# Optimization experiments

Measured on AMD Instinct MI355X. Metric: run time of the kernel, lower is better.

Reference implementation:

```python
import jax, jax.numpy as jnp
import numpy as np

B, S, H, D = 4, 2048, 12, 64
WINDOW = 128          # local_attention window => (w//2, w//2) sliding window
BASE = 16000.0        # rope theta (ProkBert default)
NEG = -1e9


def rotate_half(x):
    x1, x2 = jnp.split(x, 2, axis=-1)
    return jnp.concatenate([-x2, x1], axis=-1)


def setup_inputs() -> dict:
    key = jax.random.key(0)
    k1, = jax.random.split(key, 1)
    qkv = jax.random.normal(k1, (B, S, 3, H, D), dtype=jnp.float32)
    pos = jnp.arange(S)
    inv_freq = 1.0 / (BASE ** (jnp.arange(0, D, 2).astype(jnp.float32) / D))
    freqs = pos[:, None].astype(jnp.float32) * inv_freq[None, :]   # (S, D/2)
    emb = jnp.concatenate([freqs, freqs], axis=-1)                  # (S, D)
    cos = jnp.cos(emb)
    sin = jnp.sin(emb)
    dist = jnp.abs(pos[:, None] - pos[None, :])
    mask = jnp.where(dist <= WINDOW // 2, 0.0, NEG).astype(jnp.float32)[None, None]  # (1,1,S,S)
    return {"qkv": qkv, "cos": cos, "sin": sin, "mask": mask}


def reference(qkv, cos, sin, mask):
    # qkv: (B, S, 3, H, D) -> q/k/v: (B, H, S, D)
    q = jnp.swapaxes(qkv[:, :, 0], 1, 2)
    k = jnp.swapaxes(qkv[:, :, 1], 1, 2)
    v = jnp.swapaxes(qkv[:, :, 2], 1, 2)
    cos_b = cos[None, None]   # (1,1,S,D)
    sin_b = sin[None, None]
    q = q * cos_b + rotate_half(q) * sin_b
    k = k * cos_b + rotate_half(k) * sin_b
    scale = D ** -0.5
    scores = jnp.einsum('bhqd,bhkd->bhqk', q, k) * scale + mask
    w = jax.nn.softmax(scores.astype(jnp.float32), axis=-1).astype(q.dtype)
    out = jnp.einsum('bhqk,bhkd->bhqd', w, v)
    out = jnp.swapaxes(out, 1, 2).reshape(B, S, H * D)  # (B, S, dim)
    return out
```

## Files before the change

### kernel.cpp

```cpp
#include <hip/hip_runtime.h>
#include <hip/hip_bf16.h>
#include <cstdint>


typedef short bf16x8 __attribute__((ext_vector_type(8)));
typedef float f32x4  __attribute__((ext_vector_type(4)));
typedef uint32_t u32x4 __attribute__((ext_vector_type(4)));

#define SLEN   2048
#define NHEAD  12
#define NBATCH 4
#define HD     64
#define WHALF  64
#define QT     128
#define KROWS  256
#define NKC    9
#define VST    68
#define VROWS  136
#define QSCALE 0.18033688011112042f


__device__ __forceinline__ uint32_t cvt_pk(float lo, float hi) {
    uint32_t r;
    asm("v_cvt_pk_bf16_f32 %0, %1, %2" : "=v"(r) : "v"(lo), "v"(hi));
    return r;
}

__global__ __launch_bounds__(512, 6) void prokbert_attn(
        const float* __restrict__ qkv, const float* __restrict__ cosT,
        const float* __restrict__ sinT, float* __restrict__ out)
{
    __shared__ __align__(16) uint32_t sbuf[VROWS * VST];
    short* sKp = (short*)sbuf;

    const int tid = threadIdx.x;

    const int bid = blockIdx.x;
    const int gid = (bid & 7) * 96 + (bid >> 3);
    const int qt = gid & 15;
    const int hh = gid >> 4;
    const int h = hh % NHEAD, b = hh / NHEAD;

    const int q0 = qt * QT;
    const int kstart = q0 - WHALF;

    const int wv = tid >> 6;
    const int lane = tid & 63;
    const int r = lane & 15, g = lane >> 4;
    const int rx = r & 7;
    const int qrow = q0 + wv * 16 + r;

    const int rrb = tid >> 2, c4 = tid & 3, d0 = c4 * 8;

#define LOADK(IT, S) \
    f32x4 xl0##S, xl1##S, xh0##S, xh1##S, cc0##S, cc1##S, ss0##S, ss1##S; \
    { \
        const int s = kstart + rrb + (IT) * 128; \
        if ((unsigned)s < SLEN) { \
            const size_t kbase = (((size_t)(b * SLEN + s) * 3 + 1) * NHEAD + h) * HD; \
            const f32x4* gxl = (const f32x4*)(qkv + kbase + d0); \
            const f32x4* gxh = (const f32x4*)(qkv + kbase + d0 + 32); \
            const f32x4* gc  = (const f32x4*)(cosT + s * HD + d0); \
            const f32x4* gs  = (const f32x4*)(sinT + s * HD + d0); \
            xl0##S = gxl[0]; xl1##S = gxl[1]; \
            xh0##S = gxh[0]; xh1##S = gxh[1]; \
            cc0##S = gc[0];  cc1##S = gc[1]; \
            ss0##S = gs[0];  ss1##S = gs[1]; \
        } else { \
            const f32x4 z = {0.f, 0.f, 0.f, 0.f}; \
            xl0##S = z; xl1##S = z; xh0##S = z; xh1##S = z; \
            cc0##S = z; cc1##S = z; ss0##S = z; ss1##S = z; \
        } \
    }

#define CONVSTOREK(IT, S) \
    { \
        const int rr = rrb + (IT) * 128; \
        u32x4 klo, khi; \
         \
        klo[0] = cvt_pk(xl0##S[0] * cc0##S[0] - xh0##S[0] * ss0##S[0], \
                        xl0##S[1] * cc0##S[1] - xh0##S[1] * ss0##S[1]); \
        klo[1] = cvt_pk(xl0##S[2] * cc0##S[2] - xh0##S[2] * ss0##S[2], \
                        xl0##S[3] * cc0##S[3] - xh0##S[3] * ss0##S[3]); \
        klo[2] = cvt_pk(xl1##S[0] * cc1##S[0] - xh1##S[0] * ss1##S[0], \
                        xl1##S[1] * cc1##S[1] - xh1##S[1] * ss1##S[1]); \
        klo[3] = cvt_pk(xl1##S[2] * cc1##S[2] - xh1##S[2] * ss1##S[2], \
                        xl1##S[3] * cc1##S[3] - xh1##S[3] * ss1##S[3]); \
        khi[0] = cvt_pk(xh0##S[0] * cc0##S[0] + xl0##S[0] * ss0##S[0], \
                        xh0##S[1] * cc0##S[1] + xl0##S[1] * ss0##S[1]); \
        khi[1] = cvt_pk(xh0##S[2] * cc0##S[2] + xl0##S[2] * ss0##S[2], \
                        xh0##S[3] * cc0##S[3] + xl0##S[3] * ss0##S[3]); \
        khi[2] = cvt_pk(xh1##S[0] * cc1##S[0] + xl1##S[0] * ss1##S[0], \
                        xh1##S[1] * cc1##S[1] + xl1##S[1] * ss1##S[1]); \
        khi[3] = cvt_pk(xh1##S[2] * cc1##S[2] + xl1##S[2] * ss1##S[2], \
                        xh1##S[3] * cc1##S[3] + xl1##S[3] * ss1##S[3]); \
        const int sw = rr & 7; \
        *(u32x4*)&sKp[rr * 64 + ((c4 ^ sw) << 3)]       = klo; \
        *(u32x4*)&sKp[rr * 64 + (((c4 + 4) ^ sw) << 3)] = khi; \
    }

    {
        LOADK(0, a)
        LOADK(1, bb)
        CONVSTOREK(0, a)
        CONVSTOREK(1, bb)
    }
#undef LOADK
#undef CONVSTOREK

    bf16x8 qf0, qf1;
    {
        const size_t qb = (((size_t)(b * SLEN + qrow) * 3 + 0) * NHEAD + h) * HD;
        const f32x4* ga  = (const f32x4*)(qkv + qb + g * 8);
        const f32x4* gb  = (const f32x4*)(qkv + qb + 32 + g * 8);
        const f32x4* gc0 = (const f32x4*)(cosT + (size_t)qrow * HD + g * 8);
        const f32x4* gs0 = (const f32x4*)(sinT + (size_t)qrow * HD + g * 8);
        f32x4 qa0 = ga[0], qa1 = ga[1], qb0 = gb[0], qb1 = gb[1];
        f32x4 qc0 = gc0[0], qc1 = gc0[1], qs0 = gs0[0], qs1 = gs0[1];
        u32x4 w0, w1;
        w0[0] = cvt_pk((qa0[0] * qc0[0] - qb0[0] * qs0[0]) * QSCALE,
                       (qa0[1] * qc0[1] - qb0[1] * qs0[1]) * QSCALE);
        w0[1] = cvt_pk((qa0[2] * qc0[2] - qb0[2] * qs0[2]) * QSCALE,
                       (qa0[3] * qc0[3] - qb0[3] * qs0[3]) * QSCALE);
        w0[2] = cvt_pk((qa1[0] * qc1[0] - qb1[0] * qs1[0]) * QSCALE,
                       (qa1[1] * qc1[1] - qb1[1] * qs1[1]) * QSCALE);
        w0[3] = cvt_pk((qa1[2] * qc1[2] - qb1[2] * qs1[2]) * QSCALE,
                       (qa1[3] * qc1[3] - qb1[3] * qs1[3]) * QSCALE);
        w1[0] = cvt_pk((qb0[0] * qc0[0] + qa0[0] * qs0[0]) * QSCALE,
                       (qb0[1] * qc0[1] + qa0[1] * qs0[1]) * QSCALE);
        w1[1] = cvt_pk((qb0[2] * qc0[2] + qa0[2] * qs0[2]) * QSCALE,
                       (qb0[3] * qc0[3] + qa0[3] * qs0[3]) * QSCALE);
        w1[2] = cvt_pk((qb1[0] * qc1[0] + qa1[0] * qs1[0]) * QSCALE,
                       (qb1[1] * qc1[1] + qa1[1] * qs1[1]) * QSCALE);
        w1[3] = cvt_pk((qb1[2] * qc1[2] + qa1[2] * qs1[2]) * QSCALE,
                       (qb1[3] * qc1[3] + qa1[3] * qs1[3]) * QSCALE);
        qf0 = __builtin_bit_cast(bf16x8, w0);
        qf1 = __builtin_bit_cast(bf16x8, w1);
    }
    __syncthreads();

    f32x4 sc[NKC];
    #pragma unroll
    for (int kc = 0; kc < NKC; ++kc) {
        const int row = wv * 16 + kc * 16 + r;
        const bf16x8 ka0 = *(const bf16x8*)&sKp[row * 64 + ((g ^ rx) << 3)];
        const bf16x8 ka1 = *(const bf16x8*)&sKp[row * 64 + (((g + 4) ^ rx) << 3)];
        f32x4 c = {0.f, 0.f, 0.f, 0.f};
        c = __builtin_amdgcn_mfma_f32_16x16x32_bf16(ka0, qf0, c, 0, 0, 0);
        c = __builtin_amdgcn_mfma_f32_16x16x32_bf16(ka1, qf1, c, 0, 0, 0);
        sc[kc] = c;
    }

    const int tg = 4 * g;
    float sum = 0.f;
    #pragma unroll
    for (int kc = 0; kc < NKC; ++kc) {
        #pragma unroll
        for (int i = 0; i < 4; ++i) {
            float e = exp2f(sc[kc][i]);
            if (kc == 0) e = (tg + i >= r) ? e : 0.f;
            if (kc == 8) e = (tg + i <= r) ? e : 0.f;
            sc[kc][i] = e;
            sum += e;
        }
    }
    sum += __shfl_xor(sum, 16);
    sum += __shfl_xor(sum, 32);
    const int oob = max(0, WHALF - qrow) + max(0, qrow - (SLEN - 1 - WHALF));
    const float inv = 1.f / (sum - (float)oob);

    u32x4 paw[5];
    #pragma unroll
    for (int kb = 0; kb < 4; ++kb) {
        paw[kb][0] = cvt_pk(sc[2 * kb][0], sc[2 * kb][1]);
        paw[kb][1] = cvt_pk(sc[2 * kb][2], sc[2 * kb][3]);
        paw[kb][2] = cvt_pk(sc[2 * kb + 1][0], sc[2 * kb + 1][1]);
        paw[kb][3] = cvt_pk(sc[2 * kb + 1][2], sc[2 * kb + 1][3]);
    }
    paw[4][0] = cvt_pk(sc[8][0], sc[8][1]);
    paw[4][1] = cvt_pk(sc[8][2], sc[8][3]);
    paw[4][2] = 0; paw[4][3] = 0;

    const int vkp = tid >> 2, vdb = tid & 3, vd0 = vdb * 16;
    const int s0 = kstart + 2 * vkp, s1 = s0 + 1;
    f32x4 va[4], vb4[4];
    {
        const f32x4 z = {0.f, 0.f, 0.f, 0.f};
        if ((unsigned)s0 < SLEN) {
            const f32x4* g0 = (const f32x4*)(qkv +
                (((size_t)(b * SLEN + s0) * 3 + 2) * NHEAD + h) * HD + vd0);
            va[0] = g0[0]; va[1] = g0[1]; va[2] = g0[2]; va[3] = g0[3];
        } else { va[0] = z; va[1] = z; va[2] = z; va[3] = z; }
        if ((unsigned)s1 < SLEN) {
            const f32x4* g1 = (const f32x4*)(qkv +
                (((size_t)(b * SLEN + s1) * 3 + 2) * NHEAD + h) * HD + vd0);
            vb4[0] = g1[0]; vb4[1] = g1[1]; vb4[2] = g1[2]; vb4[3] = g1[3];
        } else { vb4[0] = z; vb4[1] = z; vb4[2] = z; vb4[3] = z; }
    }
    __syncthreads();

    #pragma unroll
    for (int u = 0; u < 4; ++u) {
        u32x4 dw;
        dw[0] = cvt_pk(va[u][0], vb4[u][0]);
        dw[1] = cvt_pk(va[u][1], vb4[u][1]);
        dw[2] = cvt_pk(va[u][2], vb4[u][2]);
        dw[3] = cvt_pk(va[u][3], vb4[u][3]);
        *(u32x4*)&sbuf[vkp * VST + vd0 + u * 4] = dw;
    }
    if (tid < 136) {
        const u32x4 z = {0, 0, 0, 0};
        *(u32x4*)&sbuf[128 * VST + tid * 4] = z;
    }
    __syncthreads();

    const uint32_t* vptr = &sbuf[(wv * 8 + 2 * g) * VST + r];
    f32x4 oacc[4] = {{0,0,0,0},{0,0,0,0},{0,0,0,0},{0,0,0,0}};
    #pragma unroll
    for (int kb = 0; kb < 5; ++kb) {
        const bf16x8 pa = __builtin_bit_cast(bf16x8, paw[kb]);
        #pragma unroll
        for (int dc = 0; dc < 4; ++dc) {
            const int base = kb * 16 * VST + dc * 16;
            u32x4 w;
            w[0] = vptr[base];
            w[1] = vptr[base + VST];
            w[2] = vptr[base + 8 * VST];
            w[3] = vptr[base + 9 * VST];
            const bf16x8 vb = __builtin_bit_cast(bf16x8, w);
            oacc[dc] = __builtin_amdgcn_mfma_f32_16x16x32_bf16(pa, vb, oacc[dc], 0, 0, 0);
        }
    }

    #pragma unroll
    for (int i = 0; i < 4; ++i) {
        const float iq = __shfl(inv, g * 4 + i);
        const int qg = q0 + wv * 16 + g * 4 + i;
        float* orow = out + (((size_t)(b * SLEN + qg)) * NHEAD + h) * HD + r;
        orow[0]  = oacc[0][i] * iq;
        orow[16] = oacc[1][i] * iq;
        orow[32] = oacc[2][i] * iq;
        orow[48] = oacc[3][i] * iq;
    }
}

extern "C" void kernel_launch(void* const* d_in, const int* in_sizes, int n_in,
                              void* d_out, int out_size, void* d_ws, size_t ws_size,
                              hipStream_t stream) {
    const float* qkv  = (const float*)d_in[0];
    const float* cosT = (const float*)d_in[1];
    const float* sinT = (const float*)d_in[2];
    float* out = (float*)d_out;
    dim3 grid(16 * NHEAD * NBATCH);
    dim3 block(512);
    hipLaunchKernelGGL(prokbert_attn, grid, block, 0, stream, qkv, cosT, sinT, out);
}
```

Before: 27.32 us.

## Halve query tile to 64 rows with 256-thread blocks and doubled grid

Shrinks each block's query tile from 128 to 64 rows (4 waves instead of 8) and doubles the grid to 1536 blocks. The K and V staging loops are reworked for 256 threads: K now takes three load/convert passes and V is loaded as 8-float chunks over three iterations. The zeroing of the padding V rows in shared memory is replaced by skipping those LDS reads in the last MFMA step. This spreads work over more, smaller blocks to improve occupancy and balance, but the K/V halo is now loaded for every 64 queries instead of every 128, so the redundant global traffic per query goes up.

Result: slower. 31.13 us (+14.0%).

```diff
diff --git a/kernel.cpp b/kernel.cpp
--- a/kernel.cpp
+++ b/kernel.cpp
@@ -12,11 +12,11 @@
 #define NBATCH 4
 #define HD     64
 #define WHALF  64
-#define QT     128
-#define KROWS  256
+#define QT     64
+#define KROWS  192
 #define NKC    9
 #define VST    68
-#define VROWS  136
+#define VROWS  96
 #define QSCALE 0.18033688011112042f
 
 
@@ -26,7 +26,7 @@
     return r;
 }
 
-__global__ __launch_bounds__(512, 6) void prokbert_attn(
+__global__ __launch_bounds__(256, 6) void prokbert_attn(
         const float* __restrict__ qkv, const float* __restrict__ cosT,
         const float* __restrict__ sinT, float* __restrict__ out)
 {
@@ -36,9 +36,9 @@
     const int tid = threadIdx.x;
 
     const int bid = blockIdx.x;
-    const int gid = (bid & 7) * 96 + (bid >> 3);
-    const int qt = gid & 15;
-    const int hh = gid >> 4;
+    const int gid = (bid & 7) * 192 + (bid >> 3);
+    const int qt = gid & 31;
+    const int hh = gid >> 5;
     const int h = hh % NHEAD, b = hh / NHEAD;
 
     const int q0 = qt * QT;
@@ -55,7 +55,7 @@
 #define LOADK(IT, S) \
     f32x4 xl0##S, xl1##S, xh0##S, xh1##S, cc0##S, cc1##S, ss0##S, ss1##S; \
     { \
-        const int s = kstart + rrb + (IT) * 128; \
+        const int s = kstart + rrb + (IT) * 64; \
         if ((unsigned)s < SLEN) { \
             const size_t kbase = (((size_t)(b * SLEN + s) * 3 + 1) * NHEAD + h) * HD; \
             const f32x4* gxl = (const f32x4*)(qkv + kbase + d0); \
@@ -75,7 +75,7 @@
 
 #define CONVSTOREK(IT, S) \
     { \
-        const int rr = rrb + (IT) * 128; \
+        const int rr = rrb + (IT) * 64; \
         u32x4 klo, khi; \
          \
         klo[0] = cvt_pk(xl0##S[0] * cc0##S[0] - xh0##S[0] * ss0##S[0], \
@@ -103,7 +103,9 @@
         LOADK(0, a)
         LOADK(1, bb)
         CONVSTOREK(0, a)
+        LOADK(2, cc)
         CONVSTOREK(1, bb)
+        CONVSTOREK(2, cc)
     }
 #undef LOADK
 #undef CONVSTOREK
@@ -181,36 +183,41 @@
     paw[4][1] = cvt_pk(sc[8][2], sc[8][3]);
     paw[4][2] = 0; paw[4][3] = 0;
 
-    const int vkp = tid >> 2, vdb = tid & 3, vd0 = vdb * 16;
-    const int s0 = kstart + 2 * vkp, s1 = s0 + 1;
-    f32x4 va[4], vb4[4];
-    {
+    f32x4 va[3][2], vb[3][2];
+    #pragma unroll
+    for (int it = 0; it < 3; ++it) {
+        const int j = tid + it * 256;
+        const int kp = j >> 3, dd = (j & 7) * 8;
+        const int s0 = kstart + 2 * kp, s1 = s0 + 1;
         const f32x4 z = {0.f, 0.f, 0.f, 0.f};
         if ((unsigned)s0 < SLEN) {
             const f32x4* g0 = (const f32x4*)(qkv +
-                (((size_t)(b * SLEN + s0) * 3 + 2) * NHEAD + h) * HD + vd0);
-            va[0] = g0[0]; va[1] = g0[1]; va[2] = g0[2]; va[3] = g0[3];
-        } else { va[0] = z; va[1] = z; va[2] = z; va[3] = z; }
+                (((size_t)(b * SLEN + s0) * 3 + 2) * NHEAD + h) * HD + dd);
+            va[it][0] = g0[0]; va[it][1] = g0[1];
+        } else { va[it][0] = z; va[it][1] = z; }
         if ((unsigned)s1 < SLEN) {
             const f32x4* g1 = (const f32x4*)(qkv +
-                (((size_t)(b * SLEN + s1) * 3 + 2) * NHEAD + h) * HD + vd0);
-            vb4[0] = g1[0]; vb4[1] = g1[1]; vb4[2] = g1[2]; vb4[3] = g1[3];
-        } else { vb4[0] = z; vb4[1] = z; vb4[2] = z; vb4[3] = z; }
+                (((size_t)(b * SLEN + s1) * 3 + 2) * NHEAD + h) * HD + dd);
+            vb[it][0] = g1[0]; vb[it][1] = g1[1];
+        } else { vb[it][0] = z; vb[it][1] = z; }
     }
     __syncthreads();
 
     #pragma unroll
-    for (int u = 0; u < 4; ++u) {
-        u32x4 dw;
-        dw[0] = cvt_pk(va[u][0], vb4[u][0]);
-        dw[1] = cvt_pk(va[u][1], vb4[u][1]);
-        dw[2] = cvt_pk(va[u][2], vb4[u][2]);
-        dw[3] = cvt_pk(va[u][3], vb4[u][3]);
-        *(u32x4*)&sbuf[vkp * VST + vd0 + u * 4] = dw;
-    }
-    if (tid < 136) {
-        const u32x4 z = {0, 0, 0, 0};
-        *(u32x4*)&sbuf[128 * VST + tid * 4] = z;
+    for (int it = 0; it < 3; ++it) {
+        const int j = tid + it * 256;
+        const int kp = j >> 3, dd = (j & 7) * 8;
+        u32x4 w0, w1;
+        w0[0] = cvt_pk(va[it][0][0], vb[it][0][0]);
+        w0[1] = cvt_pk(va[it][0][1], vb[it][0][1]);
+        w0[2] = cvt_pk(va[it][0][2], vb[it][0][2]);
+        w0[3] = cvt_pk(va[it][0][3], vb[it][0][3]);
+        w1[0] = cvt_pk(va[it][1][0], vb[it][1][0]);
+        w1[1] = cvt_pk(va[it][1][1], vb[it][1][1]);
+        w1[2] = cvt_pk(va[it][1][2], vb[it][1][2]);
+        w1[3] = cvt_pk(va[it][1][3], vb[it][1][3]);
+        *(u32x4*)&sbuf[kp * VST + dd]     = w0;
+        *(u32x4*)&sbuf[kp * VST + dd + 4] = w1;
     }
     __syncthreads();
 
@@ -225,10 +232,14 @@
             u32x4 w;
             w[0] = vptr[base];
             w[1] = vptr[base + VST];
-            w[2] = vptr[base + 8 * VST];
-            w[3] = vptr[base + 9 * VST];
-            const bf16x8 vb = __builtin_bit_cast(bf16x8, w);
-            oacc[dc] = __builtin_amdgcn_mfma_f32_16x16x32_bf16(pa, vb, oacc[dc], 0, 0, 0);
+            if (kb < 4) {
+                w[2] = vptr[base + 8 * VST];
+                w[3] = vptr[base + 9 * VST];
+            } else {
+                w[2] = 0; w[3] = 0;
+            }
+            const bf16x8 vbf = __builtin_bit_cast(bf16x8, w);
+            oacc[dc] = __builtin_amdgcn_mfma_f32_16x16x32_bf16(pa, vbf, oacc[dc], 0, 0, 0);
         }
     }
 
@@ -251,7 +262,7 @@
     const float* cosT = (const float*)d_in[1];
     const float* sinT = (const float*)d_in[2];
     float* out = (float*)d_out;
-    dim3 grid(16 * NHEAD * NBATCH);
-    dim3 block(512);
+    dim3 grid(32 * NHEAD * NBATCH);
+    dim3 block(256);
     hipLaunchKernelGGL(prokbert_attn, grid, block, 0, stream, qkv, cosT, sinT, out);
 }
```
